# Kernel optimization log

Measured on AMD Instinct MI355X. Metric: run time of the kernel, lower is better.

The kernel has to match this reference:

```python
import jax, jax.numpy as jnp
import numpy as np
import math

D = 1024
H = 16

def _new_gelu(x):
    return 0.5 * x * (1.0 + jnp.tanh(math.sqrt(2.0 / math.pi) * (x + 0.044715 * x ** 3)))

def _layer_norm(x, w):
    mu = jnp.mean(x, axis=-1, keepdims=True)
    var = jnp.var(x, axis=-1, keepdims=True)
    return (x - mu) * jax.lax.rsqrt(var + 1e-5) * w

def setup_inputs() -> dict:
    key = jax.random.key(0)
    ks = jax.random.split(key, 8)
    B, T = 2, 2048
    s = lambda fan_in: 1.0 / math.sqrt(fan_in)
    return {
        "x": jax.random.normal(ks[0], (B, T, D), jnp.float32),
        "ln1_w": jnp.ones((D,), jnp.float32),
        "attn_w": jax.random.normal(ks[1], (D, 3 * D), jnp.float32) * s(D),
        "attn_b": jnp.zeros((3 * D,), jnp.float32),
        "proj_w": jax.random.normal(ks[2], (D, D), jnp.float32) * s(D),
        "proj_b": jnp.zeros((D,), jnp.float32),
        "ln2_w": jnp.ones((D,), jnp.float32),
        "li1_w": jax.random.normal(ks[3], (D, 4 * D), jnp.float32) * s(D),
        "li1_b": jnp.zeros((4 * D,), jnp.float32),
        "li2_w": jax.random.normal(ks[4], (4 * D, D), jnp.float32) * s(4 * D),
        "li2_b": jnp.zeros((D,), jnp.float32),
    }

def reference(x, ln1_w, attn_w, attn_b, proj_w, proj_b, ln2_w, li1_w, li1_b, li2_w, li2_b):
    B, T, C = x.shape
    Dh = C // H
    # --- causal self-attention on pre-LN input ---
    h = _layer_norm(x, ln1_w)
    qkv = h @ attn_w + attn_b                      # [B,T,3C]
    q, k, v = jnp.split(qkv, 3, axis=-1)
    q = q.reshape(B, T, H, Dh)
    k = k.reshape(B, T, H, Dh)
    v = v.reshape(B, T, H, Dh)
    # NOTE: faithful to source — scale is 1/sqrt(BATCH), not 1/sqrt(head_dim)
    scale = 1.0 / math.sqrt(B)
    scores = jnp.einsum('bthd,bshd->bhts', q, k) * scale   # [B,H,T,T]
    causal = jnp.tril(jnp.ones((T, T), bool))
    scores = jnp.where(causal, scores, -jnp.inf)
    attn = jax.nn.softmax(scores, axis=-1)
    o = jnp.einsum('bhts,bshd->bthd', attn, v).reshape(B, T, C)
    x = x + o @ proj_w + proj_b
    # --- MLP ---
    h = _layer_norm(x, ln2_w)
    x = x + _new_gelu(h @ li1_w + li1_b) @ li2_w + li2_b
    return x
```

## Files before the change

### kernel.cpp

```cpp
#include <hip/hip_runtime.h>

typedef _Float16 f16;
typedef _Float16 f16x8 __attribute__((ext_vector_type(8)));
typedef _Float16 f16x4 __attribute__((ext_vector_type(4)));
typedef float    f32x4 __attribute__((ext_vector_type(4)));
typedef float    f32x16 __attribute__((ext_vector_type(16)));
typedef unsigned u32;
typedef unsigned u32x4 __attribute__((ext_vector_type(4)));

#define GAS __attribute__((address_space(1)))
#define LAS __attribute__((address_space(3)))

static __device__ __forceinline__ void gload_lds16(const void* g, void* l) {
    __builtin_amdgcn_global_load_lds((const GAS void*)g, (LAS void*)l, 16, 0, 0);
}

__global__ void wconv_t(const float* __restrict__ w, f16* __restrict__ wt, int K, int N) {
    __shared__ f16 t[32][33];
    const int tx = threadIdx.x, ty = threadIdx.y;
    const int n0 = blockIdx.x * 32, k0 = blockIdx.y * 32;
#pragma unroll
    for (int i = 0; i < 4; i++)
        t[ty + i * 8][tx] = (f16)w[(size_t)(k0 + ty + i * 8) * N + n0 + tx];
    __syncthreads();
#pragma unroll
    for (int i = 0; i < 4; i++)
        wt[(size_t)(n0 + ty + i * 8) * K + k0 + tx] = t[tx][ty + i * 8];
}

__global__ __launch_bounds__(256) void ln_kernel(const float* __restrict__ x,
                                                 const float* __restrict__ w,
                                                 f16* __restrict__ h) {
    const int row = blockIdx.x, tid = threadIdx.x;
    const float4 v = reinterpret_cast<const float4*>(x)[(size_t)row * 256 + tid];
    float s = v.x + v.y + v.z + v.w;
    float q = v.x * v.x + v.y * v.y + v.z * v.z + v.w * v.w;
#pragma unroll
    for (int m = 1; m < 64; m <<= 1) { s += __shfl_xor(s, m); q += __shfl_xor(q, m); }
    __shared__ float ss[4], qq[4];
    if ((tid & 63) == 0) { ss[tid >> 6] = s; qq[tid >> 6] = q; }
    __syncthreads();
    s = ss[0] + ss[1] + ss[2] + ss[3];
    q = qq[0] + qq[1] + qq[2] + qq[3];
    const float mu = s * (1.0f / 1024.0f);
    const float var = q * (1.0f / 1024.0f) - mu * mu;
    const float rs = rsqrtf(var + 1e-5f);
    const float4 wv = reinterpret_cast<const float4*>(w)[tid];
    f16x4 o;
    o[0] = (f16)((v.x - mu) * rs * wv.x);
    o[1] = (f16)((v.y - mu) * rs * wv.y);
    o[2] = (f16)((v.z - mu) * rs * wv.z);
    o[3] = (f16)((v.w - mu) * rs * wv.w);
    reinterpret_cast<f16x4*>(h)[(size_t)row * 256 + tid] = o;
}

__global__ __launch_bounds__(256) void vtrans(const f16* __restrict__ V, f16* __restrict__ Vt) {
    __shared__ f16 tl[64][72];
    const int tid = threadIdx.x;
    const int t0 = blockIdx.x * 64, bh = blockIdx.y;
    const int b = bh >> 4, hh = bh & 15;
    const int rr = tid >> 3, cc = (tid & 7) * 8;
#pragma unroll
    for (int p = 0; p < 2; p++) {
        f16x8 v = *(const f16x8*)(V + (size_t)(b * 2048 + t0 + p * 32 + rr) * 1024 + hh * 64 + cc);
#pragma unroll
        for (int j = 0; j < 8; j++) tl[p * 32 + rr][cc + j] = v[j];
    }
    __syncthreads();
#pragma unroll
    for (int p = 0; p < 2; p++) {
        const int d = p * 32 + rr;
        f16x8 o;
#pragma unroll
        for (int j = 0; j < 8; j++) o[j] = tl[cc + j][d];
        *(f16x8*)(Vt + (size_t)(bh * 64 + d) * 2048 + t0 + cc) = o;
    }
}

template <int EPI>
__global__ __launch_bounds__(512) void gemm_f16(
    const f16* __restrict__ A, int lda,
    const f16* __restrict__ Bt, int ldb,
    const float* __restrict__ bias,
    const float* __restrict__ res,
    void* __restrict__ outp,
    f16* __restrict__ oq, f16* __restrict__ ok, f16* __restrict__ ov,
    int N, int K) {
    __shared__ alignas(16) f16 As[3][128 * 32];
    __shared__ alignas(16) f16 Bs[3][128 * 32];
    const int tid = threadIdx.x;
    const int lane = tid & 63, wv = tid >> 6;
    const int wr = wv >> 2, wc = wv & 3;
    const int m0 = blockIdx.x * 128, n0 = blockIdx.y * 128;
    const int l15 = lane & 15, lg = lane >> 4;

    f32x4 acc[4][2] = {};

    const int ar = tid >> 2;
    const int ac = (tid & 3) * 8;
    const size_t koff = (size_t)blockIdx.z * K;
    const f16* gA = A + (size_t)(m0 + ar) * lda + ac + koff;
    const f16* gB = Bt + (size_t)(n0 + ar) * ldb + ac + koff;
    char* lA0 = (char*)As + wv * 1024;
    char* lB0 = (char*)Bs + wv * 1024;

    auto stage = [&](int buf, int k0) {
        gload_lds16(gA + k0, lA0 + buf * 8192);
        gload_lds16(gB + k0, lB0 + buf * 8192);
    };
    auto compute = [&](int buf) {
        f16x8 af[4], bf[2];
#pragma unroll
        for (int i = 0; i < 4; i++)
            af[i] = *(const f16x8*)&As[buf][(wr * 64 + i * 16 + l15) * 32 + lg * 8];
#pragma unroll
        for (int n = 0; n < 2; n++)
            bf[n] = *(const f16x8*)&Bs[buf][(wc * 32 + n * 16 + l15) * 32 + lg * 8];
#pragma unroll
        for (int mi = 0; mi < 4; mi++)
#pragma unroll
            for (int ni = 0; ni < 2; ni++)
                acc[mi][ni] = __builtin_amdgcn_mfma_f32_16x16x32_f16(af[mi], bf[ni], acc[mi][ni], 0, 0, 0);
    };

    const int nk = K >> 5;
    stage(0, 0);
    if (nk > 1) {
        stage(1, 32);
        asm volatile("s_waitcnt vmcnt(2)" ::: "memory");
    } else {
        asm volatile("s_waitcnt vmcnt(0)" ::: "memory");
    }
    __builtin_amdgcn_s_barrier();

    for (int t = 0; t < nk; ++t) {
        const bool pref = (t + 2 < nk);
        if (pref) stage((t + 2) % 3, (t + 2) * 32);
        compute(t % 3);
        if (t + 1 < nk) {
            if (pref) asm volatile("s_waitcnt vmcnt(2)" ::: "memory");
            else      asm volatile("s_waitcnt vmcnt(0)" ::: "memory");
            __builtin_amdgcn_s_barrier();
        }
    }

#pragma unroll
    for (int mi = 0; mi < 4; mi++) {
#pragma unroll
        for (int ni = 0; ni < 2; ni++) {
            const int gc = n0 + wc * 32 + ni * 16 + l15;
            const float bb = (EPI == 3) ? 0.0f : bias[gc];
#pragma unroll
            for (int r = 0; r < 4; r++) {
                const int gr = m0 + wr * 64 + mi * 16 + lg * 4 + r;
                float v = acc[mi][ni][r] + bb;
                if (EPI == 0) {
                    if (gc < 1024)      oq[(size_t)gr * 1024 + gc]        = (f16)(v * 0.70710678118654752f);
                    else if (gc < 2048) ok[(size_t)gr * 1024 + gc - 1024] = (f16)v;
                    else                ov[(size_t)gr * 1024 + gc - 2048] = (f16)v;
                } else if (EPI == 1) {
                    ((float*)outp)[(size_t)gr * N + gc] = v + res[(size_t)gr * N + gc];
                } else if (EPI == 2) {
                    const float z = 0.7978845608028654f * (v + 0.044715f * v * v * v);
                    const float t = 1.0f - 2.0f / (__builtin_amdgcn_exp2f(2.8853900817779268f * z) + 1.0f);
                    ((f16*)outp)[(size_t)gr * N + gc] = (f16)(0.5f * v * (1.0f + t));
                } else {
                    float* P = (float*)outp + (size_t)blockIdx.z * ((size_t)gridDim.x * 128) * N;
                    P[(size_t)gr * N + gc] = v;
                }
            }
        }
    }
}

__global__ __launch_bounds__(256) void kred(const float* __restrict__ p0,
                                            const float* __restrict__ p1,
                                            const float* __restrict__ bias,
                                            const float* __restrict__ res,
                                            float* __restrict__ out) {
    const size_t i = (size_t)blockIdx.x * 256 + threadIdx.x;
    const float4 a = ((const float4*)p0)[i];
    const float4 b = ((const float4*)p1)[i];
    const float4 r = ((const float4*)res)[i];
    const float4 w = ((const float4*)bias)[i & 255];
    float4 o;
    o.x = a.x + b.x + r.x + w.x;
    o.y = a.y + b.y + r.y + w.y;
    o.z = a.z + b.z + r.z + w.z;
    o.w = a.w + b.w + r.w + w.w;
    ((float4*)out)[i] = o;
}

__global__ __launch_bounds__(512) void attn_kernel(
    const f16* __restrict__ Q, const f16* __restrict__ Kb,
    const f16* __restrict__ Vt, f16* __restrict__ O) {
    __shared__ alignas(16) char pool[32768];
    const int tid = threadIdx.x, lane = tid & 63, w = tid >> 6;
    const int l31 = lane & 31, hi = lane >> 5;
    const int bx = blockIdx.x;
    const int qs = bx >> 5, bh = bx & 31;
    const int b = bh >> 4, hh = bh & 15;
    const int qtile = w * 8 + qs;
    const int q0 = qtile * 32;
    const int last = qtile >> 1;
    const int nk = ((56 + qs) >> 1) + 1;

    const f16* qrow = Q + (size_t)(b * 2048 + q0 + l31) * 1024 + hh * 64 + hi * 8;
    f16x8 qf[4];
#pragma unroll
    for (int s = 0; s < 4; s++) qf[s] = *(const f16x8*)(qrow + s * 16);

    f32x16 oacc[2] = {};
    float m = -3e38f, l = 0.0f;

    const int srow = tid >> 3, sslot = (tid & 7) ^ ((tid >> 3) & 7);
    const f16* kg = Kb + ((size_t)b * 2048 + srow) * 1024 + hh * 64 + sslot * 8;
    const f16* vg = Vt + ((size_t)bh * 64 + srow) * 2048 + sslot * 8;
    char* kld = pool + tid * 16;
    char* vld = pool + 8192 + tid * 16;

    auto stage = [&](int buf, int kt) {
        gload_lds16(kg + (size_t)kt * 65536, kld + buf * 16384);
        gload_lds16(vg + kt * 64, vld + buf * 16384);
    };

    const int rs = l31 & 7;

    auto tilestep = [&](int buf, bool diag) {
        const f16* Kbuf = (const f16*)(pool + buf * 16384);
        const f16* Vbuf = (const f16*)(pool + buf * 16384 + 8192);
        const bool doH1 = !diag || (qtile & 1);
        const int triH = qtile & 1;

        f16x8 k0[4], k1[4];
#pragma unroll
        for (int s = 0; s < 4; s++)
            k0[s] = *(const f16x8*)&Kbuf[l31 * 64 + (((s * 2 + hi) ^ rs) * 8)];
        if (doH1)
#pragma unroll
            for (int s = 0; s < 4; s++)
                k1[s] = *(const f16x8*)&Kbuf[(32 + l31) * 64 + (((s * 2 + hi) ^ rs) * 8)];

        f32x16 sacc0 = {}, sacc1 = {};
        __builtin_amdgcn_s_setprio(1);
#pragma unroll
        for (int s = 0; s < 4; s++)
            sacc0 = __builtin_amdgcn_mfma_f32_32x32x16_f16(k0[s], qf[s], sacc0, 0, 0, 0);
        if (doH1)
#pragma unroll
            for (int s = 0; s < 4; s++)
                sacc1 = __builtin_amdgcn_mfma_f32_32x32x16_f16(k1[s], qf[s], sacc1, 0, 0, 0);
        __builtin_amdgcn_s_setprio(0);

        if (diag) {
            if (triH == 0) {
#pragma unroll
                for (int r = 0; r < 16; r++) {
                    const int keyoff = (r & 3) + 8 * (r >> 2) + 4 * hi;
                    sacc0[r] = (keyoff > l31) ? -3e38f : sacc0[r];
                }
            } else {
#pragma unroll
                for (int r = 0; r < 16; r++) {
                    const int keyoff = (r & 3) + 8 * (r >> 2) + 4 * hi;
                    sacc1[r] = (keyoff > l31) ? -3e38f : sacc1[r];
                }
            }
        }
        float t8[8];
#pragma unroll
        for (int i = 0; i < 8; i++) t8[i] = fmaxf(sacc0[2 * i], sacc0[2 * i + 1]);
        if (doH1)
#pragma unroll
            for (int i = 0; i < 8; i++) t8[i] = fmaxf(t8[i], fmaxf(sacc1[2 * i], sacc1[2 * i + 1]));
#pragma unroll
        for (int i = 0; i < 4; i++) t8[i] = fmaxf(t8[i], t8[i + 4]);
        float tm = fmaxf(fmaxf(t8[0], t8[1]), fmaxf(t8[2], t8[3]));
        tm = fmaxf(tm, __shfl_xor(tm, 32));
        const bool up = tm > m + 8.0f;
        if (__any(up)) {
            const float mnew = up ? tm : m;
            const float alpha = __expf(m - mnew);
            m = mnew;
            l *= alpha;
#pragma unroll
            for (int r = 0; r < 16; r++) { oacc[0][r] *= alpha; oacc[1][r] *= alpha; }
        }
        const float mref = m * 1.44269504f;

        float psum = 0.0f;
        u32 wd[8];
        {
            float p[16];
#pragma unroll
            for (int r = 0; r < 16; r++)
                p[r] = __builtin_amdgcn_exp2f(sacc0[r] * 1.44269504f - mref);
            float s8[8];
#pragma unroll
            for (int i = 0; i < 8; i++) s8[i] = p[2 * i] + p[2 * i + 1];
#pragma unroll
            for (int i = 0; i < 4; i++) s8[i] = s8[i] + s8[i + 4];
            psum += (s8[0] + s8[1]) + (s8[2] + s8[3]);
#pragma unroll
            for (int i = 0; i < 8; i++)
                wd[i] = __builtin_bit_cast(u32, __builtin_amdgcn_cvt_pkrtz(p[2 * i], p[2 * i + 1]));
        }
        const u32 e0 = __shfl_xor(hi ? wd[0] : wd[2], 32);
        const u32 e1 = __shfl_xor(hi ? wd[1] : wd[3], 32);
        const u32 e2 = __shfl_xor(hi ? wd[4] : wd[6], 32);
        const u32 e3 = __shfl_xor(hi ? wd[5] : wd[7], 32);
        u32x4 c0, c1;
        c0[0] = hi ? e0 : wd[0]; c0[1] = hi ? e1 : wd[1];
        c0[2] = hi ? wd[2] : e0; c0[3] = hi ? wd[3] : e1;
        c1[0] = hi ? e2 : wd[4]; c1[1] = hi ? e3 : wd[5];
        c1[2] = hi ? wd[6] : e2; c1[3] = hi ? wd[7] : e3;
        const f16x8 pb00 = __builtin_bit_cast(f16x8, c0);
        const f16x8 pb01 = __builtin_bit_cast(f16x8, c1);

        f16x8 vfa, vfb;
        __builtin_amdgcn_s_setprio(1);
        vfa = *(const f16x8*)&Vbuf[l31 * 64 + ((hi ^ rs) * 8)];
        vfb = *(const f16x8*)&Vbuf[l31 * 64 + (((2 + hi) ^ rs) * 8)];
        oacc[0] = __builtin_amdgcn_mfma_f32_32x32x16_f16(vfa, pb00, oacc[0], 0, 0, 0);
        oacc[0] = __builtin_amdgcn_mfma_f32_32x32x16_f16(vfb, pb01, oacc[0], 0, 0, 0);
        vfa = *(const f16x8*)&Vbuf[(32 + l31) * 64 + ((hi ^ rs) * 8)];
        vfb = *(const f16x8*)&Vbuf[(32 + l31) * 64 + (((2 + hi) ^ rs) * 8)];
        oacc[1] = __builtin_amdgcn_mfma_f32_32x32x16_f16(vfa, pb00, oacc[1], 0, 0, 0);
        oacc[1] = __builtin_amdgcn_mfma_f32_32x32x16_f16(vfb, pb01, oacc[1], 0, 0, 0);
        __builtin_amdgcn_s_setprio(0);

        if (doH1) {
            float p[16];
#pragma unroll
            for (int r = 0; r < 16; r++)
                p[r] = __builtin_amdgcn_exp2f(sacc1[r] * 1.44269504f - mref);
            float s8[8];
#pragma unroll
            for (int i = 0; i < 8; i++) s8[i] = p[2 * i] + p[2 * i + 1];
#pragma unroll
            for (int i = 0; i < 4; i++) s8[i] = s8[i] + s8[i + 4];
            psum += (s8[0] + s8[1]) + (s8[2] + s8[3]);
#pragma unroll
            for (int i = 0; i < 8; i++)
                wd[i] = __builtin_bit_cast(u32, __builtin_amdgcn_cvt_pkrtz(p[2 * i], p[2 * i + 1]));
            const u32 f0 = __shfl_xor(hi ? wd[0] : wd[2], 32);
            const u32 f1 = __shfl_xor(hi ? wd[1] : wd[3], 32);
            const u32 f2 = __shfl_xor(hi ? wd[4] : wd[6], 32);
            const u32 f3 = __shfl_xor(hi ? wd[5] : wd[7], 32);
            u32x4 d0, d1;
            d0[0] = hi ? f0 : wd[0]; d0[1] = hi ? f1 : wd[1];
            d0[2] = hi ? wd[2] : f0; d0[3] = hi ? wd[3] : f1;
            d1[0] = hi ? f2 : wd[4]; d1[1] = hi ? f3 : wd[5];
            d1[2] = hi ? wd[6] : f2; d1[3] = hi ? wd[7] : f3;
            const f16x8 pb10 = __builtin_bit_cast(f16x8, d0);
            const f16x8 pb11 = __builtin_bit_cast(f16x8, d1);

            __builtin_amdgcn_s_setprio(1);
            vfa = *(const f16x8*)&Vbuf[l31 * 64 + (((4 + hi) ^ rs) * 8)];
            vfb = *(const f16x8*)&Vbuf[l31 * 64 + (((6 + hi) ^ rs) * 8)];
            oacc[0] = __builtin_amdgcn_mfma_f32_32x32x16_f16(vfa, pb10, oacc[0], 0, 0, 0);
            oacc[0] = __builtin_amdgcn_mfma_f32_32x32x16_f16(vfb, pb11, oacc[0], 0, 0, 0);
            vfa = *(const f16x8*)&Vbuf[(32 + l31) * 64 + (((4 + hi) ^ rs) * 8)];
            vfb = *(const f16x8*)&Vbuf[(32 + l31) * 64 + (((6 + hi) ^ rs) * 8)];
            oacc[1] = __builtin_amdgcn_mfma_f32_32x32x16_f16(vfa, pb10, oacc[1], 0, 0, 0);
            oacc[1] = __builtin_amdgcn_mfma_f32_32x32x16_f16(vfb, pb11, oacc[1], 0, 0, 0);
            __builtin_amdgcn_s_setprio(0);
        }
        psum += __shfl_xor(psum, 32);
        l += psum;
    };

    stage(0, 0);
    asm volatile("s_waitcnt vmcnt(0)" ::: "memory");
    __builtin_amdgcn_s_barrier();
    int buf = 0;
    for (int t = 0; t < nk; ++t) {
        if (t + 1 < nk) stage(buf ^ 1, t + 1);
        if (t <= last) tilestep(buf, t == last);
        asm volatile("s_waitcnt vmcnt(0)" ::: "memory");
        __builtin_amdgcn_s_barrier();
        buf ^= 1;
    }

    const float inv = 1.0f / l;
    f16* ot = (f16*)pool + (w & 3) * (32 * 72);
#pragma unroll
    for (int g = 0; g < 2; g++) {
        if ((w >> 2) == g) {
#pragma unroll
            for (int dt = 0; dt < 2; dt++)
#pragma unroll
                for (int r = 0; r < 16; r++) {
                    const int d = dt * 32 + (r & 3) + 8 * (r >> 2) + 4 * hi;
                    ot[l31 * 72 + d] = (f16)(oacc[dt][r] * inv);
                }
            asm volatile("s_waitcnt lgkmcnt(0)" ::: "memory");
#pragma unroll
            for (int i = 0; i < 4; i++) {
                const int row = i * 8 + (lane >> 3), col = (lane & 7) * 8;
                const f16x8 o8 = *(const f16x8*)&ot[row * 72 + col];
                *(f16x8*)(O + (size_t)(b * 2048 + q0 + row) * 1024 + hh * 64 + col) = o8;
            }
        }
        __syncthreads();
    }
}

extern "C" void kernel_launch(void* const* d_in, const int* in_sizes, int n_in,
                              void* d_out, int out_size, void* d_ws, size_t ws_size,
                              hipStream_t stream) {
    const float* x      = (const float*)d_in[0];
    const float* ln1_w  = (const float*)d_in[1];
    const float* attn_w = (const float*)d_in[2];
    const float* attn_b = (const float*)d_in[3];
    const float* proj_w = (const float*)d_in[4];
    const float* proj_b = (const float*)d_in[5];
    const float* ln2_w  = (const float*)d_in[6];
    const float* li1_w  = (const float*)d_in[7];
    const float* li1_b  = (const float*)d_in[8];
    const float* li2_w  = (const float*)d_in[9];
    const float* li2_b  = (const float*)d_in[10];
    float* out = (float*)d_out;

    char* ws = (char*)d_ws;
    size_t off = 0;
    auto alloc = [&](size_t bytes) { void* p = ws + off; off += (bytes + 255) & ~(size_t)255; return p; };
    f16* W1t = (f16*)alloc((size_t)3072 * 1024 * 2);
    f16* W2t = (f16*)alloc((size_t)1024 * 1024 * 2);
    f16* W3t = (f16*)alloc((size_t)4096 * 1024 * 2);
    f16* W4t = (f16*)alloc((size_t)1024 * 4096 * 2);
    f16* h   = (f16*)alloc((size_t)4096 * 1024 * 2);
    f16* Qb  = (f16*)alloc((size_t)4096 * 1024 * 2);
    f16* Kb  = (f16*)alloc((size_t)4096 * 1024 * 2);
    f16* Vb  = (f16*)alloc((size_t)4096 * 1024 * 2);
    f16* Vt  = (f16*)alloc((size_t)4096 * 1024 * 2);
    f16* Ob  = (f16*)alloc((size_t)4096 * 1024 * 2);
    float* x1 = (float*)alloc((size_t)4096 * 1024 * 4);
    float* P  = (float*)alloc((size_t)2 * 4096 * 1024 * 4);
    f16* Ab = Qb;

    dim3 b328(32, 8);
    wconv_t<<<dim3(96, 32),  b328, 0, stream>>>(attn_w, W1t, 1024, 3072);
    wconv_t<<<dim3(32, 32),  b328, 0, stream>>>(proj_w, W2t, 1024, 1024);
    wconv_t<<<dim3(128, 32), b328, 0, stream>>>(li1_w,  W3t, 1024, 4096);
    wconv_t<<<dim3(32, 128), b328, 0, stream>>>(li2_w,  W4t, 4096, 1024);

    ln_kernel<<<4096, 256, 0, stream>>>(x, ln1_w, h);
    gemm_f16<0><<<dim3(32, 24), 512, 0, stream>>>(h, 1024, W1t, 1024, attn_b, nullptr,
                                                  nullptr, Qb, Kb, Vb, 3072, 1024);
    vtrans<<<dim3(32, 32), 256, 0, stream>>>(Vb, Vt);
    attn_kernel<<<256, 512, 0, stream>>>(Qb, Kb, Vt, Ob);
    gemm_f16<1><<<dim3(32, 8), 512, 0, stream>>>(Ob, 1024, W2t, 1024, proj_b, x,
                                                 x1, nullptr, nullptr, nullptr, 1024, 1024);
    ln_kernel<<<4096, 256, 0, stream>>>(x1, ln2_w, h);
    gemm_f16<2><<<dim3(32, 32), 512, 0, stream>>>(h, 1024, W3t, 1024, li1_b, nullptr,
                                                  Ab, nullptr, nullptr, nullptr, 4096, 1024);
    gemm_f16<3><<<dim3(32, 8, 2), 512, 0, stream>>>(Ab, 4096, W4t, 4096, nullptr, nullptr,
                                                    P, nullptr, nullptr, nullptr, 1024, 2048);
    kred<<<4096, 256, 0, stream>>>(P, P + (size_t)4096 * 1024, li2_b, x1, out);
}
```

Measured before the change: 261.0 us.

## Enlarge GEMM tile to 256x128 with XOR-swizzled LDS and split-K projection

The GEMM block tile grows from 128x128 to 256x128, so each wave computes a 64x64 sub-tile (4x4 MFMAs) instead of 64x32, which raises MFMA work per LDS fragment load. The LDS layout gets an XOR swizzle on the 16-byte chunk index to reduce bank conflicts on fragment reads, and launch bounds now request 4 waves per SIMD. The attention output projection is switched to split-K over two slices plus the existing reduction kernel, which adds a partial-sum write/read pass. Grids halve along M, so each GEMM has fewer blocks, and the larger accumulator set risks register pressure and lower occupancy.

```diff
diff --git a/kernel.cpp b/kernel.cpp
--- a/kernel.cpp
+++ b/kernel.cpp
@@ -78,7 +78,7 @@
 }
 
 template <int EPI>
-__global__ __launch_bounds__(512) void gemm_f16(
+__global__ __launch_bounds__(512, 4) void gemm_f16(
     const f16* __restrict__ A, int lda,
     const f16* __restrict__ Bt, int ldb,
     const float* __restrict__ bias,
@@ -86,40 +86,43 @@
     void* __restrict__ outp,
     f16* __restrict__ oq, f16* __restrict__ ok, f16* __restrict__ ov,
     int N, int K) {
-    __shared__ alignas(16) f16 As[3][128 * 32];
+    __shared__ alignas(16) f16 As[3][256 * 32];
     __shared__ alignas(16) f16 Bs[3][128 * 32];
     const int tid = threadIdx.x;
     const int lane = tid & 63, wv = tid >> 6;
-    const int wr = wv >> 2, wc = wv & 3;
-    const int m0 = blockIdx.x * 128, n0 = blockIdx.y * 128;
+    const int wr = wv >> 1, wc = wv & 1;
+    const int m0 = blockIdx.x * 256, n0 = blockIdx.y * 128;
     const int l15 = lane & 15, lg = lane >> 4;
 
-    f32x4 acc[4][2] = {};
-
-    const int ar = tid >> 2;
-    const int ac = (tid & 3) * 8;
+    f32x4 acc[4][4] = {};
+
+    const int sr = tid >> 2;
+    const int ss = (tid & 3) ^ (sr & 3);
     const size_t koff = (size_t)blockIdx.z * K;
-    const f16* gA = A + (size_t)(m0 + ar) * lda + ac + koff;
-    const f16* gB = Bt + (size_t)(n0 + ar) * ldb + ac + koff;
-    char* lA0 = (char*)As + wv * 1024;
-    char* lB0 = (char*)Bs + wv * 1024;
+    const f16* gA  = A  + (size_t)(m0 + sr) * lda + ss * 8 + koff;
+    const f16* gA2 = gA + (size_t)128 * lda;
+    const f16* gB  = Bt + (size_t)(n0 + sr) * ldb + ss * 8 + koff;
+    char* lA = (char*)As + tid * 16;
+    char* lB = (char*)Bs + tid * 16;
 
     auto stage = [&](int buf, int k0) {
-        gload_lds16(gA + k0, lA0 + buf * 8192);
-        gload_lds16(gB + k0, lB0 + buf * 8192);
+        gload_lds16(gA  + k0, lA + buf * 16384);
+        gload_lds16(gA2 + k0, lA + buf * 16384 + 8192);
+        gload_lds16(gB  + k0, lB + buf * 8192);
     };
     auto compute = [&](int buf) {
-        f16x8 af[4], bf[2];
-#pragma unroll
-        for (int i = 0; i < 4; i++)
-            af[i] = *(const f16x8*)&As[buf][(wr * 64 + i * 16 + l15) * 32 + lg * 8];
-#pragma unroll
-        for (int n = 0; n < 2; n++)
-            bf[n] = *(const f16x8*)&Bs[buf][(wc * 32 + n * 16 + l15) * 32 + lg * 8];
+        f16x8 af[4], bf[4];
+#pragma unroll
+        for (int i = 0; i < 4; i++) {
+            const int ra = wr * 64 + i * 16 + l15;
+            af[i] = *(const f16x8*)&As[buf][ra * 32 + ((lg ^ (ra & 3)) * 8)];
+            const int rb = wc * 64 + i * 16 + l15;
+            bf[i] = *(const f16x8*)&Bs[buf][rb * 32 + ((lg ^ (rb & 3)) * 8)];
+        }
 #pragma unroll
         for (int mi = 0; mi < 4; mi++)
 #pragma unroll
-            for (int ni = 0; ni < 2; ni++)
+            for (int ni = 0; ni < 4; ni++)
                 acc[mi][ni] = __builtin_amdgcn_mfma_f32_16x16x32_f16(af[mi], bf[ni], acc[mi][ni], 0, 0, 0);
     };
 
@@ -127,7 +130,7 @@
     stage(0, 0);
     if (nk > 1) {
         stage(1, 32);
-        asm volatile("s_waitcnt vmcnt(2)" ::: "memory");
+        asm volatile("s_waitcnt vmcnt(3)" ::: "memory");
     } else {
         asm volatile("s_waitcnt vmcnt(0)" ::: "memory");
     }
@@ -138,7 +141,7 @@
         if (pref) stage((t + 2) % 3, (t + 2) * 32);
         compute(t % 3);
         if (t + 1 < nk) {
-            if (pref) asm volatile("s_waitcnt vmcnt(2)" ::: "memory");
+            if (pref) asm volatile("s_waitcnt vmcnt(3)" ::: "memory");
             else      asm volatile("s_waitcnt vmcnt(0)" ::: "memory");
             __builtin_amdgcn_s_barrier();
         }
@@ -147,8 +150,8 @@
 #pragma unroll
     for (int mi = 0; mi < 4; mi++) {
 #pragma unroll
-        for (int ni = 0; ni < 2; ni++) {
-            const int gc = n0 + wc * 32 + ni * 16 + l15;
+        for (int ni = 0; ni < 4; ni++) {
+            const int gc = n0 + wc * 64 + ni * 16 + l15;
             const float bb = (EPI == 3) ? 0.0f : bias[gc];
 #pragma unroll
             for (int r = 0; r < 4; r++) {
@@ -165,7 +168,7 @@
                     const float t = 1.0f - 2.0f / (__builtin_amdgcn_exp2f(2.8853900817779268f * z) + 1.0f);
                     ((f16*)outp)[(size_t)gr * N + gc] = (f16)(0.5f * v * (1.0f + t));
                 } else {
-                    float* P = (float*)outp + (size_t)blockIdx.z * ((size_t)gridDim.x * 128) * N;
+                    float* P = (float*)outp + (size_t)blockIdx.z * ((size_t)gridDim.x * 256) * N;
                     P[(size_t)gr * N + gc] = v;
                 }
             }
@@ -446,16 +449,17 @@
     wconv_t<<<dim3(32, 128), b328, 0, stream>>>(li2_w,  W4t, 4096, 1024);
 
     ln_kernel<<<4096, 256, 0, stream>>>(x, ln1_w, h);
-    gemm_f16<0><<<dim3(32, 24), 512, 0, stream>>>(h, 1024, W1t, 1024, attn_b, nullptr,
+    gemm_f16<0><<<dim3(16, 24), 512, 0, stream>>>(h, 1024, W1t, 1024, attn_b, nullptr,
                                                   nullptr, Qb, Kb, Vb, 3072, 1024);
     vtrans<<<dim3(32, 32), 256, 0, stream>>>(Vb, Vt);
     attn_kernel<<<256, 512, 0, stream>>>(Qb, Kb, Vt, Ob);
-    gemm_f16<1><<<dim3(32, 8), 512, 0, stream>>>(Ob, 1024, W2t, 1024, proj_b, x,
-                                                 x1, nullptr, nullptr, nullptr, 1024, 1024);
+    gemm_f16<3><<<dim3(16, 8, 2), 512, 0, stream>>>(Ob, 1024, W2t, 1024, nullptr, nullptr,
+                                                    P, nullptr, nullptr, nullptr, 1024, 512);
+    kred<<<4096, 256, 0, stream>>>(P, P + (size_t)4096 * 1024, proj_b, x, x1);
     ln_kernel<<<4096, 256, 0, stream>>>(x1, ln2_w, h);
-    gemm_f16<2><<<dim3(32, 32), 512, 0, stream>>>(h, 1024, W3t, 1024, li1_b, nullptr,
+    gemm_f16<2><<<dim3(16, 32), 512, 0, stream>>>(h, 1024, W3t, 1024, li1_b, nullptr,
                                                   Ab, nullptr, nullptr, nullptr, 4096, 1024);
-    gemm_f16<3><<<dim3(32, 8, 2), 512, 0, stream>>>(Ab, 4096, W4t, 4096, nullptr, nullptr,
+    gemm_f16<3><<<dim3(16, 8, 2), 512, 0, stream>>>(Ab, 4096, W4t, 4096, nullptr, nullptr,
                                                     P, nullptr, nullptr, nullptr, 1024, 2048);
     kred<<<4096, 256, 0, stream>>>(P, P + (size_t)4096 * 1024, li2_b, x1, out);
 }
```

After: 272.5 us. 4.4% more time.
